# Performance work log

Measured on AMD Instinct MI355X. Metric: run time of the kernel, lower is better.

The kernel has to match this reference:

```python
import jax, jax.numpy as jnp
import numpy as np
import math

B, S, D, H = 4, 2048, 1024, 16
HD = D // H

def setup_inputs() -> dict:
    key = jax.random.key(0)
    ks = jax.random.split(key, 12)
    sc = 1.0 / math.sqrt(D)
    inp = {
        'q': jax.random.normal(ks[0], (B, S, D), jnp.float32),
        'k': jax.random.normal(ks[1], (B, S, D), jnp.float32),
        'v': jax.random.normal(ks[2], (B, S, D), jnp.float32),
        # causal mask: 1.0 where attention is disallowed (j > i)
        'mask': jnp.broadcast_to(jnp.triu(jnp.ones((S, S), jnp.float32), k=1), (B, S, S)),
        'Wq': jax.random.normal(ks[3], (D, D), jnp.float32) * sc,
        'bq': jnp.zeros((D,), jnp.float32),
        'Wk': jax.random.normal(ks[4], (D, D), jnp.float32) * sc,
        'bk': jnp.zeros((D,), jnp.float32),
        'Wv': jax.random.normal(ks[5], (D, D), jnp.float32) * sc,
        'bv': jnp.zeros((D,), jnp.float32),
        'Wo': jax.random.normal(ks[6], (D, D), jnp.float32) * sc,
        'bo': jnp.zeros((D,), jnp.float32),
    }
    return inp

def reference(q, k, v, mask, Wq, bq, Wk, bk, Wv, bv, Wo, bo):
    # linear projections (torch Linear: x @ W^T + b)
    qp = q @ Wq.T + bq
    kp = k @ Wk.T + bk
    vp = v @ Wv.T + bv
    # split heads: [B,S,D] -> [B,H,S,hd]
    qh = qp.reshape(B, S, H, HD).transpose(0, 2, 1, 3)
    kh = kp.reshape(B, S, H, HD).transpose(0, 2, 1, 3)
    vh = vp.reshape(B, S, H, HD).transpose(0, 2, 1, 3)
    scores = jnp.einsum('bhqd,bhkd->bhqk', qh, kh) / jnp.sqrt(jnp.float32(HD))
    scores = scores + mask[:, None, :, :] * jnp.float32(-100000.0)
    attn = jax.nn.softmax(scores, axis=-1)
    out = jnp.einsum('bhqk,bhkd->bhqd', attn, vh)
    out = out.transpose(0, 2, 1, 3).reshape(B, S, D)
    out = out @ Wo.T + bo
    return (out, kh, vh)
```

## Files before the change

kernel.cpp:

```cpp
#include <hip/hip_runtime.h>
#include <stdint.h>

#define Bn 4
#define Sn 2048
#define Dn 1024
#define Hn 16
#define HDn 64

typedef unsigned short u16;
typedef unsigned int u32;
typedef __attribute__((ext_vector_type(8))) __bf16 bf16x8;
typedef __attribute__((ext_vector_type(4))) float f32x4;
typedef __attribute__((ext_vector_type(16))) float f32x16;
typedef __attribute__((ext_vector_type(4))) u32 u32x4;

#define CEXP 0.18033688011112042f

#define EXP2F(x) __builtin_amdgcn_exp2f(x)

__device__ __forceinline__ u16 f2bf(float f) {
  union { float f; u32 u; } x; x.f = f;
  u32 r = x.u + 0x7FFFu + ((x.u >> 16) & 1u);
  return (u16)(r >> 16);
}

__device__ __forceinline__ void gload16(const u16* g, u16* l) {
  __builtin_amdgcn_global_load_lds(
      (const __attribute__((address_space(1))) void*)g,
      (__attribute__((address_space(3))) void*)l, 16, 0, 0);
}

__global__ void cvt_kernel(const float* __restrict__ in, u16* __restrict__ out, int n4) {
  int i = blockIdx.x * 256 + threadIdx.x;
  if (i < n4) {
    float4 v = ((const float4*)in)[i];
    ushort4 o;
    o.x = f2bf(v.x); o.y = f2bf(v.y); o.z = f2bf(v.z); o.w = f2bf(v.w);
    ((ushort4*)out)[i] = o;
  }
}

template<int MODE>
__global__ __launch_bounds__(256, 2) void gemm_bt(
    const u16* __restrict__ A, const u16* __restrict__ W,
    const float* __restrict__ bias,
    float* __restrict__ outF, u16* __restrict__ outB)
{
  __shared__ u16 As[2][4096];
  __shared__ u16 Bs[2][4096];

  const int t = threadIdx.x, w = t >> 6, lane = t & 63;
  int bid = (int)blockIdx.x;
  bid = (bid & 7) * 64 + (bid >> 3);
  const int m0 = (bid >> 3) * 128, n0 = (bid & 7) * 128;
  const int wm = (w >> 1) * 64, wn = (w & 1) * 64;
  const int lrow = lane & 15;

  f32x4 acc[4][4] = {};

  auto stage = [&](int buf, int k0) {
    #pragma unroll
    for (int i = 0; i < 2; ++i) {
      const int c = i * 256 + t;
      const int row = c >> 2;
      const int off = ((c & 3) ^ (row & 3)) * 8;
      gload16(A + (size_t)(m0 + row) * 1024 + k0 + off, &As[buf][(c & ~63) * 8]);
      gload16(W + (size_t)(n0 + row) * 1024 + k0 + off, &Bs[buf][(c & ~63) * 8]);
    }
  };

  stage(0, 0);
  for (int kt = 0; kt < 32; ++kt) {
    const int buf = kt & 1;
    __syncthreads();
    if (kt < 31) stage(buf ^ 1, (kt + 1) * 32);
    bf16x8 a[4], b[4];
    #pragma unroll
    for (int i = 0; i < 4; ++i) {
      const int ra = wm + i * 16 + lrow;
      const int rb = wn + i * 16 + lrow;
      a[i] = *(const bf16x8*)&As[buf][ra * 32 + (((lane >> 4) ^ (ra & 3)) * 8)];
      b[i] = *(const bf16x8*)&Bs[buf][rb * 32 + (((lane >> 4) ^ (rb & 3)) * 8)];
    }
    #pragma unroll
    for (int i = 0; i < 4; ++i)
      #pragma unroll
      for (int j = 0; j < 4; ++j)
        acc[i][j] = __builtin_amdgcn_mfma_f32_16x16x32_bf16(a[i], b[j], acc[i][j], 0, 0, 0);
  }

  const int g4 = (lane >> 4) * 4;
  #pragma unroll
  for (int i = 0; i < 4; ++i) {
    #pragma unroll
    for (int j = 0; j < 4; ++j) {
      const int gn = n0 + wn + j * 16 + lrow;
      const float bv = bias[gn];
      #pragma unroll
      for (int r = 0; r < 4; ++r) {
        const int gm = m0 + wm + i * 16 + g4 + r;
        const float x = acc[i][j][r] + bv;
        if (MODE == 3) {
          outF[(size_t)gm * 1024 + gn] = x;
        } else {
          const int b_ = gm >> 11, s_ = gm & 2047, h_ = gn >> 6, d_ = gn & 63;
          const size_t hidx = (((size_t)b_ * Hn + h_) * Sn + s_) * HDn + d_;
          if (MODE == 0) outB[hidx] = f2bf(x * CEXP);
          if (MODE == 1) { outF[hidx] = x; outB[hidx] = f2bf(x); }
          if (MODE == 2) { outF[hidx] = x;
                           outB[(((size_t)b_ * Hn + h_) * HDn + d_) * Sn + s_] = f2bf(x); }
        }
      }
    }
  }
}

__global__ __launch_bounds__(256, 2) void attn_kernel(
    const u16* __restrict__ qh, const u16* __restrict__ kh,
    const u16* __restrict__ vt, u16* __restrict__ ao)
{
  __shared__ u16 Ks[2][4096];
  __shared__ u16 Vs[2][4096];

  const int t = threadIdx.x, w = t >> 6, lane = t & 63;
  int bid = (int)blockIdx.x;
  bid = (bid & 7) * 64 + (bid >> 3);
  const int pr = bid & 7, bh = bid >> 3;
  const int l31 = lane & 31, h = lane >> 5;
  const int cxor = l31 & 7;

  const u16* Kb = kh + (size_t)bh * Sn * HDn;
  const u16* Vb = vt + (size_t)bh * HDn * Sn;
  const u16* Qb = qh + (size_t)bh * Sn * HDn;

  const int q0A = pr * 128 + w * 32;
  const int q0B = (15 - pr) * 128 + w * 32;
  const int qA = q0A + l31, qB = q0B + l31;

  bf16x8 qfA[4], qfB[4];
  #pragma unroll
  for (int kk = 0; kk < 4; ++kk) {
    qfA[kk] = *(const bf16x8*)(Qb + (size_t)qA * HDn + kk * 16 + h * 8);
    qfB[kk] = *(const bf16x8*)(Qb + (size_t)qB * HDn + kk * 16 + h * 8);
  }

  float mA = -1e30f, lA = 0.f, mB = -1e30f, lB = 0.f;
  f32x16 oA0 = {}, oA1 = {}, oB0 = {}, oB1 = {};

  const int NT = 2 * (16 - pr);
  const int jAmax = (q0A + 31) >> 6, jBmax = (q0B + 31) >> 6;

  auto stageKV = [&](int buf, int j0) {
    #pragma unroll
    for (int i = 0; i < 2; ++i) {
      const int c = i * 256 + t;
      const int row = c >> 3;
      const int off = (c & 7) ^ (row & 7);
      gload16(Kb + (size_t)(j0 + row) * HDn + off * 8, &Ks[buf][(c & ~63) * 8]);
      gload16(Vb + (size_t)row * Sn + j0 + off * 8, &Vs[buf][(c & ~63) * 8]);
    }
  };

  auto unit = [&](const bf16x8* qf, float& m, float& l, f32x16& o0, f32x16& o1,
                  int buf, int jt, int q0w, int qg) {
    const u16* Kbuf = &Ks[buf][0];
    const u16* Vbuf = &Vs[buf][0];
    f32x16 s0 = {}, s1 = {};

    __builtin_amdgcn_s_setprio(1);
    #pragma unroll
    for (int kk = 0; kk < 4; ++kk) {
      const int ch = ((kk * 2 + h) ^ cxor) * 8;
      bf16x8 k0 = *(const bf16x8*)&Kbuf[l31 * 64 + ch];
      bf16x8 k1 = *(const bf16x8*)&Kbuf[(32 + l31) * 64 + ch];
      s0 = __builtin_amdgcn_mfma_f32_32x32x16_bf16(k0, qf[kk], s0, 0, 0, 0);
      s1 = __builtin_amdgcn_mfma_f32_32x32x16_bf16(k1, qf[kk], s1, 0, 0, 0);
    }
    __builtin_amdgcn_s_setprio(0);

    if (jt * 64 + 63 > q0w) {
      const int kvb = jt * 64 + 4 * h;
      #pragma unroll
      for (int r = 0; r < 16; ++r) {
        const int rho = (r & 3) + 8 * (r >> 2);
        s0[r] = (kvb + rho > qg) ? -1e30f : s0[r];
        s1[r] = (kvb + 32 + rho > qg) ? -1e30f : s1[r];
      }
    }

    float mx = s0[0];
    #pragma unroll
    for (int r = 1; r < 16; ++r) mx = fmaxf(mx, s0[r]);
    #pragma unroll
    for (int r = 0; r < 16; ++r) mx = fmaxf(mx, s1[r]);
    mx = fmaxf(mx, __shfl_xor(mx, 32, 64));

    if (__any(mx > m + 11.5415603f)) {
      const float mn = fmaxf(m, mx);
      const float al = EXP2F(m - mn);
      m = mn; l *= al;
      #pragma unroll
      for (int r = 0; r < 16; ++r) { o0[r] *= al; o1[r] *= al; }
    }

    float sum = 0.f;
    #pragma unroll
    for (int r = 0; r < 16; ++r) { s0[r] = EXP2F(s0[r] - m); sum += s0[r]; }
    #pragma unroll
    for (int r = 0; r < 16; ++r) { s1[r] = EXP2F(s1[r] - m); sum += s1[r]; }
    sum += __shfl_xor(sum, 32, 64);
    l += sum;

    u32 w0[8], w1[8];
    #pragma unroll
    for (int i = 0; i < 8; ++i) {
      asm("v_cvt_pk_bf16_f32 %0, %1, %2" : "=v"(w0[i]) : "v"(s0[2 * i]), "v"(s0[2 * i + 1]));
      asm("v_cvt_pk_bf16_f32 %0, %1, %2" : "=v"(w1[i]) : "v"(s1[2 * i]), "v"(s1[2 * i + 1]));
    }
    asm("v_permlane32_swap_b32 %0, %1" : "+v"(w0[0]), "+v"(w0[2]));
    asm("v_permlane32_swap_b32 %0, %1" : "+v"(w0[1]), "+v"(w0[3]));
    asm("v_permlane32_swap_b32 %0, %1" : "+v"(w0[4]), "+v"(w0[6]));
    asm("v_permlane32_swap_b32 %0, %1" : "+v"(w0[5]), "+v"(w0[7]));
    asm("v_permlane32_swap_b32 %0, %1" : "+v"(w1[0]), "+v"(w1[2]));
    asm("v_permlane32_swap_b32 %0, %1" : "+v"(w1[1]), "+v"(w1[3]));
    asm("v_permlane32_swap_b32 %0, %1" : "+v"(w1[4]), "+v"(w1[6]));
    asm("v_permlane32_swap_b32 %0, %1" : "+v"(w1[5]), "+v"(w1[7]));

    __builtin_amdgcn_s_setprio(1);
    #pragma unroll
    for (int s = 0; s < 4; ++s) {
      const u32* wt = (s < 2) ? w0 : w1;
      const int j4 = (s & 1) * 4;
      u32x4 fr = { wt[j4], wt[j4 + 1], wt[j4 + 2], wt[j4 + 3] };
      bf16x8 pf = __builtin_bit_cast(bf16x8, fr);
      const int ch = ((2 * s + h) ^ cxor) * 8;
      bf16x8 v0 = *(const bf16x8*)&Vbuf[l31 * 64 + ch];
      bf16x8 v1 = *(const bf16x8*)&Vbuf[(32 + l31) * 64 + ch];
      o0 = __builtin_amdgcn_mfma_f32_32x32x16_bf16(v0, pf, o0, 0, 0, 0);
      o1 = __builtin_amdgcn_mfma_f32_32x32x16_bf16(v1, pf, o1, 0, 0, 0);
    }
    __builtin_amdgcn_s_setprio(0);
  };

  stageKV(0, 0);
  for (int jt = 0; jt < NT; ++jt) {
    const int buf = jt & 1;
    __syncthreads();
    if (jt + 1 < NT) stageKV(buf ^ 1, (jt + 1) * 64);
    if (jt <= jBmax) unit(qfB, mB, lB, oB0, oB1, buf, jt, q0B, qB);
    if (jt <= jAmax) unit(qfA, mA, lA, oA0, oA1, buf, jt, q0A, qA);
  }

  const int b_ = bh >> 4, h_ = bh & 15;
  {
    const float rl = 1.0f / lA;
    u16* base = ao + ((size_t)b_ * Sn + qA) * Dn + h_ * HDn;
    #pragma unroll
    for (int n = 0; n < 2; ++n)
      #pragma unroll
      for (int u = 0; u < 4; ++u) {
        const f32x16& o = n ? oA1 : oA0;
        ushort4 ov;
        ov.x = f2bf(o[4 * u + 0] * rl); ov.y = f2bf(o[4 * u + 1] * rl);
        ov.z = f2bf(o[4 * u + 2] * rl); ov.w = f2bf(o[4 * u + 3] * rl);
        *(ushort4*)&base[n * 32 + 8 * u + 4 * h] = ov;
      }
  }
  {
    const float rl = 1.0f / lB;
    u16* base = ao + ((size_t)b_ * Sn + qB) * Dn + h_ * HDn;
    #pragma unroll
    for (int n = 0; n < 2; ++n)
      #pragma unroll
      for (int u = 0; u < 4; ++u) {
        const f32x16& o = n ? oB1 : oB0;
        ushort4 ov;
        ov.x = f2bf(o[4 * u + 0] * rl); ov.y = f2bf(o[4 * u + 1] * rl);
        ov.z = f2bf(o[4 * u + 2] * rl); ov.w = f2bf(o[4 * u + 3] * rl);
        *(ushort4*)&base[n * 32 + 8 * u + 4 * h] = ov;
      }
  }
}

extern "C" void kernel_launch(void* const* d_in, const int* in_sizes, int n_in,
                              void* d_out, int out_size, void* d_ws, size_t ws_size,
                              hipStream_t stream)
{
  const float* q  = (const float*)d_in[0];
  const float* k  = (const float*)d_in[1];
  const float* v  = (const float*)d_in[2];
  const float* Wq = (const float*)d_in[4];
  const float* bq = (const float*)d_in[5];
  const float* Wk = (const float*)d_in[6];
  const float* bk = (const float*)d_in[7];
  const float* Wv = (const float*)d_in[8];
  const float* bv = (const float*)d_in[9];
  const float* Wo = (const float*)d_in[10];
  const float* bo = (const float*)d_in[11];

  float* out_o  = (float*)d_out;
  float* out_kh = out_o + (size_t)Bn * Sn * Dn;
  float* out_vh = out_kh + (size_t)Bn * Sn * Dn;

  char* ws = (char*)d_ws;
  const size_t MB = 1ull << 20;
  u16* wq_bf = (u16*)(ws + 0 * MB);
  u16* wk_bf = (u16*)(ws + 2 * MB);
  u16* wv_bf = (u16*)(ws + 4 * MB);
  u16* wo_bf = (u16*)(ws + 6 * MB);
  u16* q_bf  = (u16*)(ws + 8 * MB);
  u16* k_bf  = (u16*)(ws + 24 * MB);
  u16* v_bf  = (u16*)(ws + 40 * MB);
  u16* qh_bf = (u16*)(ws + 56 * MB);
  u16* kh_bf = (u16*)(ws + 72 * MB);
  u16* vt_bf = (u16*)(ws + 88 * MB);
  u16* ao_bf = q_bf;

  const int NC = Bn * Sn * Dn / 4;
  cvt_kernel<<<NC / 256, 256, 0, stream>>>(q, q_bf, NC);
  cvt_kernel<<<NC / 256, 256, 0, stream>>>(k, k_bf, NC);
  cvt_kernel<<<NC / 256, 256, 0, stream>>>(v, v_bf, NC);
  const int NW = Dn * Dn / 4;
  cvt_kernel<<<NW / 256, 256, 0, stream>>>(Wq, wq_bf, NW);
  cvt_kernel<<<NW / 256, 256, 0, stream>>>(Wk, wk_bf, NW);
  cvt_kernel<<<NW / 256, 256, 0, stream>>>(Wv, wv_bf, NW);
  cvt_kernel<<<NW / 256, 256, 0, stream>>>(Wo, wo_bf, NW);

  gemm_bt<0><<<512, 256, 0, stream>>>(q_bf, wq_bf, bq, nullptr, qh_bf);
  gemm_bt<1><<<512, 256, 0, stream>>>(k_bf, wk_bf, bk, out_kh, kh_bf);
  gemm_bt<2><<<512, 256, 0, stream>>>(v_bf, wv_bf, bv, out_vh, vt_bf);

  attn_kernel<<<512, 256, 0, stream>>>(qh_bf, kh_bf, vt_bf, ao_bf);

  gemm_bt<3><<<512, 256, 0, stream>>>(ao_bf, wo_bf, bo, out_o, nullptr);
}
```

Before: 223.4 us.

## Split attention into one query tile per block and batch conversion launches

The attention kernel now gives each block a single 128-row query tile instead of a pair of mirrored tiles. This doubles the grid to 1024 blocks and raises the launch-bounds occupancy hint to 4. The LDS layout for K/V changes from XOR-swizzled rows to a fragment-ordered layout, so MFMA operand reads are contiguous per lane, and staging uses precomputed source pointers. The seven separate fp32-to-bf16 conversion launches are merged into two launches that use blockIdx.y to pick the tensor. The trade-off is that load balance across the causal triangle now depends on block scheduling rather than pairing, and each block reuses the K/V tiles it stages for only one query tile.

```diff
diff --git a/kernel.cpp b/kernel.cpp
--- a/kernel.cpp
+++ b/kernel.cpp
@@ -30,14 +30,32 @@
       (__attribute__((address_space(3))) void*)l, 16, 0, 0);
 }
 
-__global__ void cvt_kernel(const float* __restrict__ in, u16* __restrict__ out, int n4) {
+__global__ void cvt3_kernel(const float* __restrict__ a, const float* __restrict__ b,
+                            const float* __restrict__ c,
+                            u16* __restrict__ oa, u16* __restrict__ ob,
+                            u16* __restrict__ oc) {
+  const float* in = (blockIdx.y == 0) ? a : (blockIdx.y == 1) ? b : c;
+  u16* out = (blockIdx.y == 0) ? oa : (blockIdx.y == 1) ? ob : oc;
   int i = blockIdx.x * 256 + threadIdx.x;
-  if (i < n4) {
-    float4 v = ((const float4*)in)[i];
-    ushort4 o;
-    o.x = f2bf(v.x); o.y = f2bf(v.y); o.z = f2bf(v.z); o.w = f2bf(v.w);
-    ((ushort4*)out)[i] = o;
-  }
+  float4 v = ((const float4*)in)[i];
+  ushort4 o;
+  o.x = f2bf(v.x); o.y = f2bf(v.y); o.z = f2bf(v.z); o.w = f2bf(v.w);
+  ((ushort4*)out)[i] = o;
+}
+
+__global__ void cvt4_kernel(const float* __restrict__ a, const float* __restrict__ b,
+                            const float* __restrict__ c, const float* __restrict__ d,
+                            u16* __restrict__ oa, u16* __restrict__ ob,
+                            u16* __restrict__ oc, u16* __restrict__ od) {
+  const float* in = (blockIdx.y == 0) ? a : (blockIdx.y == 1) ? b
+                   : (blockIdx.y == 2) ? c : d;
+  u16* out = (blockIdx.y == 0) ? oa : (blockIdx.y == 1) ? ob
+            : (blockIdx.y == 2) ? oc : od;
+  int i = blockIdx.x * 256 + threadIdx.x;
+  float4 v = ((const float4*)in)[i];
+  ushort4 o;
+  o.x = f2bf(v.x); o.y = f2bf(v.y); o.z = f2bf(v.z); o.w = f2bf(v.w);
+  ((ushort4*)out)[i] = o;
 }
 
 template<int MODE>
@@ -115,7 +133,7 @@
   }
 }
 
-__global__ __launch_bounds__(256, 2) void attn_kernel(
+__global__ __launch_bounds__(256, 4) void attn_kernel(
     const u16* __restrict__ qh, const u16* __restrict__ kh,
     const u16* __restrict__ vt, u16* __restrict__ ao)
 {
@@ -123,46 +141,47 @@
   __shared__ u16 Vs[2][4096];
 
   const int t = threadIdx.x, w = t >> 6, lane = t & 63;
-  int bid = (int)blockIdx.x;
-  bid = (bid & 7) * 64 + (bid >> 3);
-  const int pr = bid & 7, bh = bid >> 3;
+  const int bid = (int)blockIdx.x;
+  const int ii = bid & 127, qq = ii >> 5, j = ii & 31;
+  const int bh = (bid >> 7) * 8 + (j >> 2);
+  const int p = 4 * qq + ((j + qq) & 3);
   const int l31 = lane & 31, h = lane >> 5;
-  const int cxor = l31 & 7;
 
   const u16* Kb = kh + (size_t)bh * Sn * HDn;
   const u16* Vb = vt + (size_t)bh * HDn * Sn;
   const u16* Qb = qh + (size_t)bh * Sn * HDn;
 
-  const int q0A = pr * 128 + w * 32;
-  const int q0B = (15 - pr) * 128 + w * 32;
-  const int qA = q0A + l31, qB = q0B + l31;
-
-  bf16x8 qfA[4], qfB[4];
+  const int q0w = p * 128 + w * 32;
+  const int qg = q0w + l31;
+  const int NT = 2 * p + 2;
+  const int NTw = ((q0w + 31) >> 6) + 1;
+
+  bf16x8 qf[4];
   #pragma unroll
-  for (int kk = 0; kk < 4; ++kk) {
-    qfA[kk] = *(const bf16x8*)(Qb + (size_t)qA * HDn + kk * 16 + h * 8);
-    qfB[kk] = *(const bf16x8*)(Qb + (size_t)qB * HDn + kk * 16 + h * 8);
-  }
-
-  float mA = -1e30f, lA = 0.f, mB = -1e30f, lB = 0.f;
-  f32x16 oA0 = {}, oA1 = {}, oB0 = {}, oB1 = {};
-
-  const int NT = 2 * (16 - pr);
-  const int jAmax = (q0A + 31) >> 6, jBmax = (q0B + 31) >> 6;
-
-  auto stageKV = [&](int buf, int j0) {
-    #pragma unroll
-    for (int i = 0; i < 2; ++i) {
-      const int c = i * 256 + t;
-      const int row = c >> 3;
-      const int off = (c & 7) ^ (row & 7);
-      gload16(Kb + (size_t)(j0 + row) * HDn + off * 8, &Ks[buf][(c & ~63) * 8]);
-      gload16(Vb + (size_t)row * Sn + j0 + off * 8, &Vs[buf][(c & ~63) * 8]);
-    }
+  for (int kk = 0; kk < 4; ++kk)
+    qf[kk] = *(const bf16x8*)(Qb + (size_t)qg * HDn + kk * 16 + h * 8);
+
+  float m = -1e30f, l = 0.f;
+  f32x16 o0 = {}, o1 = {};
+
+  const int c0 = t, c1 = t + 256;
+  const int kr0 = ((c0 >> 8) << 5) + (c0 & 31), kr1 = ((c1 >> 8) << 5) + (c1 & 31);
+  const u16* kSrc0 = Kb + (size_t)kr0 * HDn + ((c0 >> 6) & 3) * 16 + ((c0 >> 5) & 1) * 8;
+  const u16* kSrc1 = Kb + (size_t)kr1 * HDn + ((c1 >> 6) & 3) * 16 + ((c1 >> 5) & 1) * 8;
+  const u16* vSrc0 = Vb + (size_t)kr0 * Sn + (2 * ((c0 >> 6) & 3) + ((c0 >> 5) & 1)) * 8;
+  const u16* vSrc1 = Vb + (size_t)kr1 * Sn + (2 * ((c1 >> 6) & 3) + ((c1 >> 5) & 1)) * 8;
+  const int d0 = (c0 & ~63) * 8, d1 = (c1 & ~63) * 8;
+
+  auto stage = [&](int buf) {
+    gload16(kSrc0, &Ks[buf][d0]);
+    gload16(kSrc1, &Ks[buf][d1]);
+    gload16(vSrc0, &Vs[buf][d0]);
+    gload16(vSrc1, &Vs[buf][d1]);
+    kSrc0 += 64 * HDn; kSrc1 += 64 * HDn;
+    vSrc0 += 64;       vSrc1 += 64;
   };
 
-  auto unit = [&](const bf16x8* qf, float& m, float& l, f32x16& o0, f32x16& o1,
-                  int buf, int jt, int q0w, int qg) {
+  auto unit = [&](int buf, int jt) {
     const u16* Kbuf = &Ks[buf][0];
     const u16* Vbuf = &Vs[buf][0];
     f32x16 s0 = {}, s1 = {};
@@ -170,9 +189,8 @@
     __builtin_amdgcn_s_setprio(1);
     #pragma unroll
     for (int kk = 0; kk < 4; ++kk) {
-      const int ch = ((kk * 2 + h) ^ cxor) * 8;
-      bf16x8 k0 = *(const bf16x8*)&Kbuf[l31 * 64 + ch];
-      bf16x8 k1 = *(const bf16x8*)&Kbuf[(32 + l31) * 64 + ch];
+      bf16x8 k0 = *(const bf16x8*)&Kbuf[(kk * 64 + lane) * 8];
+      bf16x8 k1 = *(const bf16x8*)&Kbuf[((4 + kk) * 64 + lane) * 8];
       s0 = __builtin_amdgcn_mfma_f32_32x32x16_bf16(k0, qf[kk], s0, 0, 0, 0);
       s1 = __builtin_amdgcn_mfma_f32_32x32x16_bf16(k1, qf[kk], s1, 0, 0, 0);
     }
@@ -233,53 +251,35 @@
       const int j4 = (s & 1) * 4;
       u32x4 fr = { wt[j4], wt[j4 + 1], wt[j4 + 2], wt[j4 + 3] };
       bf16x8 pf = __builtin_bit_cast(bf16x8, fr);
-      const int ch = ((2 * s + h) ^ cxor) * 8;
-      bf16x8 v0 = *(const bf16x8*)&Vbuf[l31 * 64 + ch];
-      bf16x8 v1 = *(const bf16x8*)&Vbuf[(32 + l31) * 64 + ch];
+      bf16x8 v0 = *(const bf16x8*)&Vbuf[(s * 64 + lane) * 8];
+      bf16x8 v1 = *(const bf16x8*)&Vbuf[((4 + s) * 64 + lane) * 8];
       o0 = __builtin_amdgcn_mfma_f32_32x32x16_bf16(v0, pf, o0, 0, 0, 0);
       o1 = __builtin_amdgcn_mfma_f32_32x32x16_bf16(v1, pf, o1, 0, 0, 0);
     }
     __builtin_amdgcn_s_setprio(0);
   };
 
-  stageKV(0, 0);
+  stage(0);
   for (int jt = 0; jt < NT; ++jt) {
     const int buf = jt & 1;
     __syncthreads();
-    if (jt + 1 < NT) stageKV(buf ^ 1, (jt + 1) * 64);
-    if (jt <= jBmax) unit(qfB, mB, lB, oB0, oB1, buf, jt, q0B, qB);
-    if (jt <= jAmax) unit(qfA, mA, lA, oA0, oA1, buf, jt, q0A, qA);
+    if (jt + 1 < NT) stage(buf ^ 1);
+    if (jt < NTw) unit(buf, jt);
   }
 
   const int b_ = bh >> 4, h_ = bh & 15;
-  {
-    const float rl = 1.0f / lA;
-    u16* base = ao + ((size_t)b_ * Sn + qA) * Dn + h_ * HDn;
-    #pragma unroll
-    for (int n = 0; n < 2; ++n)
-      #pragma unroll
-      for (int u = 0; u < 4; ++u) {
-        const f32x16& o = n ? oA1 : oA0;
-        ushort4 ov;
-        ov.x = f2bf(o[4 * u + 0] * rl); ov.y = f2bf(o[4 * u + 1] * rl);
-        ov.z = f2bf(o[4 * u + 2] * rl); ov.w = f2bf(o[4 * u + 3] * rl);
-        *(ushort4*)&base[n * 32 + 8 * u + 4 * h] = ov;
-      }
-  }
-  {
-    const float rl = 1.0f / lB;
-    u16* base = ao + ((size_t)b_ * Sn + qB) * Dn + h_ * HDn;
-    #pragma unroll
-    for (int n = 0; n < 2; ++n)
-      #pragma unroll
-      for (int u = 0; u < 4; ++u) {
-        const f32x16& o = n ? oB1 : oB0;
-        ushort4 ov;
-        ov.x = f2bf(o[4 * u + 0] * rl); ov.y = f2bf(o[4 * u + 1] * rl);
-        ov.z = f2bf(o[4 * u + 2] * rl); ov.w = f2bf(o[4 * u + 3] * rl);
-        *(ushort4*)&base[n * 32 + 8 * u + 4 * h] = ov;
-      }
-  }
+  const float rl = 1.0f / l;
+  u16* base = ao + ((size_t)b_ * Sn + qg) * Dn + h_ * HDn;
+  #pragma unroll
+  for (int n = 0; n < 2; ++n)
+    #pragma unroll
+    for (int u = 0; u < 4; ++u) {
+      const f32x16& o = n ? o1 : o0;
+      ushort4 ov;
+      ov.x = f2bf(o[4 * u + 0] * rl); ov.y = f2bf(o[4 * u + 1] * rl);
+      ov.z = f2bf(o[4 * u + 2] * rl); ov.w = f2bf(o[4 * u + 3] * rl);
+      *(ushort4*)&base[n * 32 + 8 * u + 4 * h] = ov;
+    }
 }
 
 extern "C" void kernel_launch(void* const* d_in, const int* in_sizes, int n_in,
@@ -317,20 +317,16 @@
   u16* ao_bf = q_bf;
 
   const int NC = Bn * Sn * Dn / 4;
-  cvt_kernel<<<NC / 256, 256, 0, stream>>>(q, q_bf, NC);
-  cvt_kernel<<<NC / 256, 256, 0, stream>>>(k, k_bf, NC);
-  cvt_kernel<<<NC / 256, 256, 0, stream>>>(v, v_bf, NC);
+  cvt3_kernel<<<dim3(NC / 256, 3), 256, 0, stream>>>(q, k, v, q_bf, k_bf, v_bf);
   const int NW = Dn * Dn / 4;
-  cvt_kernel<<<NW / 256, 256, 0, stream>>>(Wq, wq_bf, NW);
-  cvt_kernel<<<NW / 256, 256, 0, stream>>>(Wk, wk_bf, NW);
-  cvt_kernel<<<NW / 256, 256, 0, stream>>>(Wv, wv_bf, NW);
-  cvt_kernel<<<NW / 256, 256, 0, stream>>>(Wo, wo_bf, NW);
+  cvt4_kernel<<<dim3(NW / 256, 4), 256, 0, stream>>>(Wq, Wk, Wv, Wo,
+                                                     wq_bf, wk_bf, wv_bf, wo_bf);
 
   gemm_bt<0><<<512, 256, 0, stream>>>(q_bf, wq_bf, bq, nullptr, qh_bf);
   gemm_bt<1><<<512, 256, 0, stream>>>(k_bf, wk_bf, bk, out_kh, kh_bf);
   gemm_bt<2><<<512, 256, 0, stream>>>(v_bf, wv_bf, bv, out_vh, vt_bf);
 
-  attn_kernel<<<512, 256, 0, stream>>>(qh_bf, kh_bf, vt_bf, ao_bf);
+  attn_kernel<<<1024, 256, 0, stream>>>(qh_bf, kh_bf, vt_bf, ao_bf);
 
   gemm_bt<3><<<512, 256, 0, stream>>>(ao_bf, wo_bf, bo, out_o, nullptr);
 }
```

Result: slower. 236.4 us (+5.8%).
